# Kernel optimization log

Measured on AMD Instinct MI355X. Metric: run time of the kernel, lower is better.

The kernel has to match this reference:

```python
import jax, jax.numpy as jnp
import numpy as np

K = 20          # neighbors
EPS = 1e-5      # BatchNorm eps (eval mode, running_mean=0, running_var=1)
SLOPE = 0.01    # LeakyReLU default negative_slope


def lrelu(v):
    return jnp.where(v >= 0, v, SLOPE * v)


def bn4d(y, g, b):  # y: (B, C, N, k) or (B, C, N)
    shape = (1, g.shape[0]) + (1,) * (y.ndim - 2)
    return y * (g / jnp.sqrt(1.0 + EPS)).reshape(shape) + b.reshape(shape)


def knn_idx(x, k):  # x: (B, C, N) -> (B, N, k) indices of k nearest points
    xx = jnp.sum(x * x, axis=1)                      # (B, N)
    inner = jnp.einsum('bcn,bcm->bnm', x, x)         # (B, N, N)
    dist = 2.0 * inner - xx[:, :, None] - xx[:, None, :]  # = -||xi-xj||^2
    _, idx = jax.lax.top_k(dist, k)
    return idx


def graph_feature(x, k):  # x: (B, C, N) -> (B, 2C, N, k)
    idx = knn_idx(x, k)                              # (B, N, k)
    xt = jnp.transpose(x, (0, 2, 1))                 # (B, N, C)
    nbr = jax.vmap(lambda p, i: p[i])(xt, idx)       # (B, N, k, C) gather
    ctr = xt[:, :, None, :]                          # (B, N, 1, C)
    feat = jnp.concatenate([nbr - ctr, jnp.broadcast_to(ctr, nbr.shape)], axis=-1)
    return jnp.transpose(feat, (0, 3, 1, 2))         # (B, 2C, N, k)


def edge_conv(x, w, g, b, bias=None):  # 1x1 conv + BN(eval) + LeakyReLU + max over k
    f = graph_feature(x, K)                          # (B, 2C, N, k)
    y = jnp.einsum('oc,bcnk->bonk', w, f)
    if bias is not None:
        y = y + bias.reshape(1, -1, 1, 1)
    return jnp.max(lrelu(bn4d(y, g, b)), axis=-1)    # (B, O, N)


def setup_inputs() -> dict:
    key = jax.random.key(0)
    ks = jax.random.split(key, 24)
    W = lambda k_, o, c: jax.random.normal(k_, (o, c), jnp.float32) / np.sqrt(c)
    g = lambda k_, c: 1.0 + 0.1 * jax.random.normal(k_, (c,), jnp.float32)
    bt = lambda k_, c: 0.1 * jax.random.normal(k_, (c,), jnp.float32)
    return {
        'x': jax.random.normal(ks[0], (8, 1024, 3), jnp.float32),
        'conv1_w': W(ks[1], 64, 6), 'conv1_b': bt(ks[2], 64),
        'bn1_g': g(ks[3], 64), 'bn1_b': bt(ks[4], 64),
        'conv2_w': W(ks[5], 64, 128), 'bn2_g': g(ks[6], 64), 'bn2_b': bt(ks[7], 64),
        'conv3_w': W(ks[8], 128, 128), 'bn3_g': g(ks[9], 128), 'bn3_b': bt(ks[10], 128),
        'conv4_w': W(ks[11], 256, 256), 'bn4_g': g(ks[12], 256), 'bn4_b': bt(ks[13], 256),
        'conv5_w': W(ks[14], 1024, 512),
        'lin1_w': W(ks[15], 512, 1024), 'bn6_g': g(ks[16], 512), 'bn6_b': bt(ks[17], 512),
        'lin2_w': W(ks[18], 256, 512), 'lin2_b': bt(ks[19], 256),
        'bn7_g': g(ks[20], 256), 'bn7_b': bt(ks[21], 256),
        'lin3_w': W(ks[22], 40, 256), 'lin3_b': bt(ks[23], 40),
    }


def reference(x, conv1_w, conv1_b, bn1_g, bn1_b, conv2_w, bn2_g, bn2_b,
              conv3_w, bn3_g, bn3_b, conv4_w, bn4_g, bn4_b, conv5_w,
              lin1_w, bn6_g, bn6_b, lin2_w, lin2_b, bn7_g, bn7_b, lin3_w, lin3_b):
    p = jnp.transpose(x, (0, 2, 1))                  # (B, 3, N)
    x1 = edge_conv(p, conv1_w, bn1_g, bn1_b, bias=conv1_b)   # (B, 64, N)
    x2 = edge_conv(x1, conv2_w, bn2_g, bn2_b)                # (B, 64, N)
    x3 = edge_conv(x2, conv3_w, bn3_g, bn3_b)                # (B, 128, N)
    x4 = edge_conv(x3, conv4_w, bn4_g, bn4_b)                # (B, 256, N)
    xc = jnp.concatenate([x1, x2, x3, x4], axis=1)           # (B, 512, N)
    e = jnp.einsum('oc,bcn->bon', conv5_w, xc)               # (B, 1024, N); bn5 unused in original forward
    gpool = jnp.max(e, axis=-1)                              # (B, 1024) adaptive_max_pool1d(1)
    y = gpool @ lin1_w.T
    y = lrelu(y * (bn6_g / jnp.sqrt(1.0 + EPS)) + bn6_b)     # dropout = identity (eval)
    y = y @ lin2_w.T + lin2_b
    y = lrelu(y * (bn7_g / jnp.sqrt(1.0 + EPS)) + bn7_b)
    return y @ lin3_w.T + lin3_b                             # (B, num_classes)
```

## Files before the change

### kernel.cpp

```cpp
#include <hip/hip_runtime.h>
#include <cmath>
#include <cstdint>
#include <cstddef>

#define NB 8
#define NPTS 1024
#define BN (NB*NPTS)
#define KNN 20
#define XC_C 512
#define BN_SC 0.99999500003749973f

static __device__ __forceinline__ float lrelu(float z) { return z >= 0.f ? z : 0.01f * z; }

template<int CTRL>
static __device__ __forceinline__ void dpp_max2(unsigned& loA, unsigned& hiA,
                                                unsigned& loB, unsigned& hiB) {
    unsigned tlA = (unsigned)__builtin_amdgcn_update_dpp(0, (int)loA, CTRL, 0xF, 0xF, false);
    unsigned thA = (unsigned)__builtin_amdgcn_update_dpp(0, (int)hiA, CTRL, 0xF, 0xF, false);
    unsigned tlB = (unsigned)__builtin_amdgcn_update_dpp(0, (int)loB, CTRL, 0xF, 0xF, false);
    unsigned thB = (unsigned)__builtin_amdgcn_update_dpp(0, (int)hiB, CTRL, 0xF, 0xF, false);
    unsigned long long a = ((unsigned long long)hiA << 32) | loA;
    unsigned long long b = ((unsigned long long)thA << 32) | tlA;
    if (b > a) { loA = tlA; hiA = thA; }
    unsigned long long c = ((unsigned long long)hiB << 32) | loB;
    unsigned long long d = ((unsigned long long)thB << 32) | tlB;
    if (d > c) { loB = tlB; hiB = thB; }
}

static __device__ __forceinline__ void wave_max_u64_x2(unsigned long long vA, unsigned long long vB,
                                                       unsigned long long& winA, unsigned long long& winB) {
    unsigned loA = (unsigned)vA, hiA = (unsigned)(vA >> 32);
    unsigned loB = (unsigned)vB, hiB = (unsigned)(vB >> 32);
    dpp_max2<0x121>(loA, hiA, loB, hiB);
    dpp_max2<0x122>(loA, hiA, loB, hiB);
    dpp_max2<0x124>(loA, hiA, loB, hiB);
    dpp_max2<0x128>(loA, hiA, loB, hiB);
    dpp_max2<0x142>(loA, hiA, loB, hiB);
    dpp_max2<0x143>(loA, hiA, loB, hiB);
    unsigned wloA = (unsigned)__builtin_amdgcn_readlane((int)loA, 63);
    unsigned whiA = (unsigned)__builtin_amdgcn_readlane((int)hiA, 63);
    unsigned wloB = (unsigned)__builtin_amdgcn_readlane((int)loB, 63);
    unsigned whiB = (unsigned)__builtin_amdgcn_readlane((int)hiB, 63);
    winA = ((unsigned long long)whiA << 32) | wloA;
    winB = ((unsigned long long)whiB << 32) | wloB;
}

static __device__ __forceinline__ unsigned long long shflx64(unsigned long long v, int m) {
    int lo = __shfl_xor((int)(unsigned)v, m);
    int hi = __shfl_xor((int)(unsigned)(v >> 32), m);
    return ((unsigned long long)(unsigned)hi << 32) | (unsigned)lo;
}

static __device__ __forceinline__ unsigned long long rdlane64(unsigned long long v, int l) {
    unsigned lo = (unsigned)__builtin_amdgcn_readlane((int)(unsigned)v, l);
    unsigned hi = (unsigned)__builtin_amdgcn_readlane((int)(unsigned)(v >> 32), l);
    return ((unsigned long long)hi << 32) | lo;
}

static __device__ __forceinline__ void bitonic64_desc_x2(unsigned long long& vA,
                                                         unsigned long long& vB, int lane) {
#pragma unroll
    for (int k = 2; k <= 64; k <<= 1) {
#pragma unroll
        for (int j = k >> 1; j > 0; j >>= 1) {
            unsigned long long pA = shflx64(vA, j);
            unsigned long long pB = shflx64(vB, j);
            bool takeMax = (((lane & k) == 0) == ((lane & j) == 0));
            vA = ((pA > vA) == takeMax) ? pA : vA;
            vB = ((pB > vB) == takeMax) ? pB : vB;
        }
    }
}

static __device__ __forceinline__ void select_pair(const float4* accA, const float4* accB,
                                                   const float4* nm4, int lane,
                                                   unsigned long long (*cw)[64],
                                                   int rA, int rB, int* __restrict__ idx) {
    unsigned long long keyA[16], keyB[16];
#pragma unroll
    for (int j = 0; j < 4; j++) {
        float4 nm = nm4[lane + 64*j];
#pragma unroll
        for (int q = 0; q < 4; q++) {
            int m = 4*(lane + 64*j) + q;
            float fA = 2.f * (&accA[j].x)[q] - (&nm.x)[q];
            unsigned uA = __float_as_uint(fA);
            unsigned sA_ = (unsigned)((int)uA >> 31);
            uA ^= (sA_ | 0x80000000u);
            keyA[4*j+q] = ((unsigned long long)uA << 32) | (unsigned)(1023 - m);
            float fB = 2.f * (&accB[j].x)[q] - (&nm.x)[q];
            unsigned uB = __float_as_uint(fB);
            unsigned sB_ = (unsigned)((int)uB >> 31);
            uB ^= (sB_ | 0x80000000u);
            keyB[4*j+q] = ((unsigned long long)uB << 32) | (unsigned)(1023 - m);
        }
    }

    unsigned long long hA = keyA[0], hB = keyB[0];
#pragma unroll
    for (int i = 1; i < 16; i++) {
        hA = keyA[i] > hA ? keyA[i] : hA;
        hB = keyB[i] > hB ? keyB[i] : hB;
    }

    unsigned long long shA = hA, shB = hB;
    bitonic64_desc_x2(shA, shB, lane);
    unsigned long long LA = rdlane64(shA, KNN - 1);
    unsigned long long LB = rdlane64(shB, KNN - 1);

    int cA = 0, cB = 0;
#pragma unroll
    for (int i = 0; i < 16; i++) {
        cA += (keyA[i] >= LA) ? 1 : 0;
        cB += (keyB[i] >= LB) ? 1 : 0;
    }
    int sA = cA, sB = cB;
#pragma unroll
    for (int off = 1; off < 64; off <<= 1) {
        int tA = __shfl_up(sA, off);
        int tB = __shfl_up(sB, off);
        if (lane >= off) { sA += tA; sB += tB; }
    }
    int totA = __builtin_amdgcn_readlane(sA, 63);
    int totB = __builtin_amdgcn_readlane(sB, 63);
    int pA = sA - cA, pB = sB - cB;

    if (totA <= 64 && totB <= 64) {
        int wa = pA, wb = pB;
#pragma unroll
        for (int i = 0; i < 16; i++) {
            if (keyA[i] >= LA) cw[0][wa++] = keyA[i];
            if (keyB[i] >= LB) cw[1][wb++] = keyB[i];
        }
        asm volatile("s_waitcnt lgkmcnt(0)" ::: "memory");
        unsigned long long vA = 0ull, vB = 0ull;
        if (lane < totA) vA = cw[0][lane];
        if (lane < totB) vB = cw[1][lane];
        bitonic64_desc_x2(vA, vB, lane);
        if (lane < KNN) {
            idx[rA * KNN + lane] = 1023 - (int)(unsigned)vA;
            idx[rB * KNN + lane] = 1023 - (int)(unsigned)vB;
        }
    } else {
#pragma unroll
        for (int ksz = 2; ksz <= 16; ksz <<= 1) {
#pragma unroll
            for (int jst = ksz >> 1; jst > 0; jst >>= 1) {
#pragma unroll
                for (int i = 0; i < 16; i++) {
                    int l = i ^ jst;
                    if (l > i) {
                        bool dsc = (i & ksz) == 0;
                        unsigned long long a = keyA[i], bbv = keyA[l];
                        bool swA = dsc ? (a < bbv) : (a > bbv);
                        if (swA) { keyA[i] = bbv; keyA[l] = a; }
                        unsigned long long c = keyB[i], d = keyB[l];
                        bool swB = dsc ? (c < d) : (c > d);
                        if (swB) { keyB[i] = d; keyB[l] = c; }
                    }
                }
            }
        }
        int mineA = 0, mineB = 0;
        for (int kk = 0; kk < KNN; kk++) {
            unsigned long long winA, winB;
            wave_max_u64_x2(keyA[0], keyB[0], winA, winB);
            if (lane == kk) {
                mineA = 1023 - (int)(unsigned)winA;
                mineB = 1023 - (int)(unsigned)winB;
            }
            bool popA = (keyA[0] == winA);
            bool popB = (keyB[0] == winB);
#pragma unroll
            for (int t = 0; t < 15; t++) {
                keyA[t] = popA ? keyA[t+1] : keyA[t];
                keyB[t] = popB ? keyB[t+1] : keyB[t];
            }
            keyA[15] = popA ? 0ull : keyA[15];
            keyB[15] = popB ? 0ull : keyB[15];
        }
        if (lane < KNN) {
            idx[rA * KNN + lane] = mineA;
            idx[rB * KNN + lane] = mineB;
        }
    }
}

static __device__ __forceinline__ unsigned short f2bf(float f) {
    unsigned u = __float_as_uint(f);
    unsigned r = u + 0x7fffu + ((u >> 16) & 1u);
    return (unsigned short)(r >> 16);
}
static __device__ __forceinline__ float bf2f(unsigned short h) {
    return __uint_as_float(((unsigned)h) << 16);
}

typedef __attribute__((ext_vector_type(8))) short short8;
typedef __attribute__((ext_vector_type(4))) float floatx4;

__global__ void prep_k(const float* __restrict__ x, float* __restrict__ ft, float* __restrict__ nrm) {
    int i = blockIdx.x * 256 + threadIdx.x;
    if (i >= BN) return;
    int b = i >> 10, n = i & 1023;
    float a = x[3*i], c = x[3*i+1], d = x[3*i+2];
    float* fb = ft + (size_t)b * 3 * NPTS;
    fb[n] = a; fb[NPTS + n] = c; fb[2*NPTS + n] = d;
    nrm[i] = a*a + c*c + d*d;
}

template<int C, int R>
__global__ __launch_bounds__(256, 2) void knn_k(const float* __restrict__ ft,
                                                const float* __restrict__ frow, int frs,
                                                const float* __restrict__ nrm,
                                                int* __restrict__ idx) {
    __shared__ unsigned long long cand[4][2][64];
    __shared__ float sbuf[2 * 4 * NPTS];
    int tid = threadIdx.x;
    int w = tid >> 6;
    int lane = tid & 63;
    int b    = blockIdx.x & 7;
    int slot = blockIdx.x >> 3;
    int r0 = b * NPTS + slot * (4*R) + R * w;
    const float* ftb = ft + (size_t)b * C * NPTS;

    float4 acc[R][4];
#pragma unroll
    for (int rr = 0; rr < R; rr++)
#pragma unroll
        for (int j = 0; j < 4; j++) acc[rr][j] = make_float4(0.f,0.f,0.f,0.f);

    if constexpr ((C & 3) == 0) {
        constexpr int NC = C / 4;
        const float4* cr0 = (const float4*)(frow + (size_t)r0 * frs);
        int frs4 = frs >> 2;
        const float4* src4 = (const float4*)ftb;
        float* sbase = &sbuf[0];
        float4 pf[4];
#pragma unroll
        for (int i = 0; i < 4; i++) pf[i] = src4[i*256 + tid];
        {
            float4* sw = (float4*)sbase;
#pragma unroll
            for (int i = 0; i < 4; i++) sw[i*256 + tid] = pf[i];
        }
        __syncthreads();
        for (int c4 = 0; c4 < NC; c4++) {
            int cur = c4 & 1;
            if (c4 + 1 < NC) {
#pragma unroll
                for (int i = 0; i < 4; i++) pf[i] = src4[(size_t)(4*(c4+1)+i)*256 + tid];
            }
            float4 ct[R];
#pragma unroll
            for (int rr = 0; rr < R; rr++) ct[rr] = cr0[c4 + rr*frs4];
            const float4* sc = (const float4*)(sbase + cur * 4 * NPTS);
#pragma unroll
            for (int cc = 0; cc < 4; cc++) {
                const float4* rm = sc + cc*256;
#pragma unroll
                for (int j = 0; j < 4; j++) {
                    float4 v = rm[lane + 64*j];
#pragma unroll
                    for (int rr = 0; rr < R; rr++) {
                        float cs = (&ct[rr].x)[cc];
                        acc[rr][j].x = fmaf(cs, v.x, acc[rr][j].x);
                        acc[rr][j].y = fmaf(cs, v.y, acc[rr][j].y);
                        acc[rr][j].z = fmaf(cs, v.z, acc[rr][j].z);
                        acc[rr][j].w = fmaf(cs, v.w, acc[rr][j].w);
                    }
                }
            }
            if (c4 + 1 < NC) {
                float4* sw = (float4*)(sbase + (cur ^ 1) * 4 * NPTS);
#pragma unroll
                for (int i = 0; i < 4; i++) sw[i*256 + tid] = pf[i];
                __syncthreads();
            }
        }
    } else {
        for (int c = 0; c < C; c++) {
            float ct[R];
#pragma unroll
            for (int rr = 0; rr < R; rr++) ct[rr] = frow[(size_t)(r0+rr) * frs + c];
            const float4* rm = (const float4*)(ftb + (size_t)c * NPTS);
#pragma unroll
            for (int j = 0; j < 4; j++) {
                float4 v = rm[lane + 64*j];
#pragma unroll
                for (int rr = 0; rr < R; rr++) {
                    float cs = ct[rr];
                    acc[rr][j].x = fmaf(cs, v.x, acc[rr][j].x);
                    acc[rr][j].y = fmaf(cs, v.y, acc[rr][j].y);
                    acc[rr][j].z = fmaf(cs, v.z, acc[rr][j].z);
                    acc[rr][j].w = fmaf(cs, v.w, acc[rr][j].w);
                }
            }
        }
    }

    const float4* nm4 = (const float4*)(nrm + b * NPTS);
#pragma unroll
    for (int p = 0; p < R/2; p++)
        select_pair(acc[2*p], acc[2*p+1], nm4, lane, cand[w], r0 + 2*p, r0 + 2*p + 1, idx);
}

template<int C, int O, bool HASB, int RPB>
__global__ void hc_k(const float* __restrict__ F, int FS,
                     const float* __restrict__ w, const float* __restrict__ bias,
                     float* __restrict__ Ht, float* __restrict__ Ct) {
    int r0 = blockIdx.x * RPB;
    int o = threadIdx.x;
    const float* wr = w + (size_t)o * (2*C);
    float h[RPB], a2[RPB];
#pragma unroll
    for (int nn = 0; nn < RPB; nn++) { h[nn] = 0.f; a2[nn] = 0.f; }
    if constexpr ((C & 3) == 0) {
        const float4* w1 = (const float4*)wr;
        const float4* w2 = (const float4*)(wr + C);
#pragma unroll 4
        for (int c4 = 0; c4 < C/4; c4++) {
            float4 wa = w1[c4], wb = w2[c4];
#pragma unroll
            for (int nn = 0; nn < RPB; nn++) {
                float4 f = *(const float4*)(F + (size_t)(r0+nn)*FS + 4*c4);
                h[nn]  = fmaf(wa.x,f.x, fmaf(wa.y,f.y, fmaf(wa.z,f.z, fmaf(wa.w,f.w, h[nn]))));
                a2[nn] = fmaf(wb.x,f.x, fmaf(wb.y,f.y, fmaf(wb.z,f.z, fmaf(wb.w,f.w, a2[nn]))));
            }
        }
    } else {
        for (int c = 0; c < C; c++) {
            float wa = wr[c], wb = wr[C+c];
#pragma unroll
            for (int nn = 0; nn < RPB; nn++) {
                float f = F[(size_t)(r0+nn)*FS + c];
                h[nn]  = fmaf(wa, f, h[nn]);
                a2[nn] = fmaf(wb, f, a2[nn]);
            }
        }
    }
    float bs = 0.f;
    if constexpr (HASB) bs = bias[o];
#pragma unroll
    for (int nn = 0; nn < RPB; nn++) {
        size_t ro = (size_t)(r0+nn)*O + o;
        Ht[ro] = h[nn];
        Ct[ro] = a2[nn] - h[nn] + bs;
    }
}

template<int O, bool WFT>
__global__ void gmax_k(const float* __restrict__ Ht, const float* __restrict__ Ct,
                       const int* __restrict__ idx,
                       const float* __restrict__ g, const float* __restrict__ bb,
                       float* __restrict__ xcs, float* __restrict__ ft, float* __restrict__ nrm) {
    int b = blockIdx.x & 7;
    int n = blockIdx.x >> 3;
    int r = b * NPTS + n;
    int o = threadIdx.x;
    const int* id = idx + r * KNN;
    float vmax = -INFINITY, vmin = INFINITY;
    const float* hb = Ht + (size_t)b * NPTS * O + o;
#pragma unroll 4
    for (int k = 0; k < KNN; k++) {
        int m = id[k];
        float v = hb[(size_t)m * O];
        vmax = fmaxf(vmax, v); vmin = fminf(vmin, v);
    }
    float ct = Ct[(size_t)r * O + o];
    float s = g[o] * BN_SC;
    float pre = (s >= 0.f ? vmax : vmin) + ct;
    float out = lrelu(fmaf(s, pre, bb[o]));
    xcs[(size_t)r * XC_C + o] = out;
    if constexpr (WFT) {
        ft[((size_t)b * O + o) * NPTS + n] = out;
        float sq = out * out;
#pragma unroll
        for (int off = 32; off > 0; off >>= 1) sq += __shfl_xor(sq, off);
        __shared__ float red[O/64 > 0 ? O/64 : 1];
        if ((o & 63) == 0) red[o >> 6] = sq;
        __syncthreads();
        if (o == 0) {
            float t = 0.f;
#pragma unroll
            for (int i = 0; i < O/64; i++) t += red[i];
            nrm[r] = t;
        }
    }
}

__global__ void xcvt_k(const float* __restrict__ xc,
                       unsigned short* __restrict__ xh, unsigned short* __restrict__ xl) {
    int i = blockIdx.x * 256 + threadIdx.x;
    float v = xc[i];
    unsigned short h = f2bf(v);
    xh[i] = h;
    xl[i] = f2bf(v - bf2f(h));
}

__global__ void wcvt_k(const float* __restrict__ w5,
                       unsigned short* __restrict__ wh, unsigned short* __restrict__ wl) {
    int i = blockIdx.x * 256 + threadIdx.x;
    float v = w5[i];
    unsigned short h = f2bf(v);
    wh[i] = h;
    wl[i] = f2bf(v - bf2f(h));
}

__global__ __launch_bounds__(256) void conv5mfma_k(const unsigned short* __restrict__ xh,
                                                   const unsigned short* __restrict__ xl,
                                                   const unsigned short* __restrict__ wh,
                                                   const unsigned short* __restrict__ wl,
                                                   float* __restrict__ part) {
    __shared__ short ah_s[32*72];
    __shared__ short al_s[32*72];
    __shared__ short bh_s[128*72];
    __shared__ short bl_s[128*72];
    int b = blockIdx.z, og = blockIdx.y, nt = blockIdx.x;
    int tid = threadIdx.x;
    int w = tid >> 6, lane = tid & 63;
    int m = lane & 15, quad = lane >> 4;
    int h = w >> 1, q = w & 1;
    size_t nbase = (size_t)b * NPTS + nt * 32;
    int obase = og * 128;
    int srow = tid >> 3;
    int scol = (tid & 7) * 8;

    floatx4 acc[4];
#pragma unroll
    for (int t = 0; t < 4; t++) acc[t] = (floatx4){0.f, 0.f, 0.f, 0.f};

    for (int kc = 0; kc < 512; kc += 64) {
        __syncthreads();
        *(short8*)(ah_s + srow*72 + scol) = *(const short8*)(xh + (nbase + srow)*512 + kc + scol);
        *(short8*)(al_s + srow*72 + scol) = *(const short8*)(xl + (nbase + srow)*512 + kc + scol);
#pragma unroll
        for (int i = 0; i < 4; i++) {
            int r = srow + i*32;
            *(short8*)(bh_s + r*72 + scol) = *(const short8*)(wh + (size_t)(obase + r)*512 + kc + scol);
            *(short8*)(bl_s + r*72 + scol) = *(const short8*)(wl + (size_t)(obase + r)*512 + kc + scol);
        }
        __syncthreads();
#pragma unroll
        for (int kk = 0; kk < 2; kk++) {
            short8 ah8 = *(const short8*)(ah_s + (h*16 + m)*72 + kk*32 + quad*8);
            short8 al8 = *(const short8*)(al_s + (h*16 + m)*72 + kk*32 + quad*8);
#pragma unroll
            for (int t = 0; t < 4; t++) {
                short8 bh8 = *(const short8*)(bh_s + (q*64 + t*16 + m)*72 + kk*32 + quad*8);
                short8 bl8 = *(const short8*)(bl_s + (q*64 + t*16 + m)*72 + kk*32 + quad*8);
                acc[t] = __builtin_amdgcn_mfma_f32_16x16x32_bf16(ah8, bh8, acc[t], 0, 0, 0);
                acc[t] = __builtin_amdgcn_mfma_f32_16x16x32_bf16(ah8, bl8, acc[t], 0, 0, 0);
                acc[t] = __builtin_amdgcn_mfma_f32_16x16x32_bf16(al8, bh8, acc[t], 0, 0, 0);
            }
        }
    }
#pragma unroll
    for (int t = 0; t < 4; t++) {
        float v = fmaxf(fmaxf(acc[t][0], acc[t][1]), fmaxf(acc[t][2], acc[t][3]));
        v = fmaxf(v, __shfl_xor(v, 16));
        v = fmaxf(v, __shfl_xor(v, 32));
        if (quad == 0)
            part[((size_t)b * 64 + nt*2 + h) * 1024 + obase + q*64 + t*16 + m] = v;
    }
}

__global__ void gpool_k(const float* __restrict__ part, float* __restrict__ gp) {
    int i = blockIdx.x * 256 + threadIdx.x;
    int b = i >> 10, o = i & 1023;
    const float* pb = part + (size_t)b * 64 * 1024 + o;
    float m = pb[0];
#pragma unroll 4
    for (int j = 1; j < 64; j++) m = fmaxf(m, pb[(size_t)j * 1024]);
    gp[i] = m;
}

template<int C, bool HASBIAS, bool ACT>
__global__ __launch_bounds__(256) void lin_k(const float* __restrict__ X, int xs,
                                             const float* __restrict__ W,
                                             const float* __restrict__ bias,
                                             const float* __restrict__ g, const float* __restrict__ bb,
                                             float* __restrict__ Y, int ys) {
    int wid = (blockIdx.x * 256 + threadIdx.x) >> 6;
    int lane = threadIdx.x & 63;
    int o = wid >> 3;
    int b = wid & 7;
    const float4* wr = (const float4*)(W + (size_t)o * C);
    const float4* xr = (const float4*)(X + (size_t)b * xs);
    float acc = 0.f;
#pragma unroll
    for (int i = 0; i < C/256; i++) {
        float4 w = wr[lane + 64*i];
        float4 xv = xr[lane + 64*i];
        acc = fmaf(w.x,xv.x, fmaf(w.y,xv.y, fmaf(w.z,xv.z, fmaf(w.w,xv.w, acc))));
    }
#pragma unroll
    for (int off = 32; off > 0; off >>= 1) acc += __shfl_xor(acc, off);
    if (lane == 0) {
        if constexpr (HASBIAS) acc += bias[o];
        if constexpr (ACT) acc = lrelu(fmaf(acc, g[o] * BN_SC, bb[o]));
        Y[(size_t)b * ys + o] = acc;
    }
}

extern "C" void kernel_launch(void* const* d_in, const int* in_sizes, int n_in,
                              void* d_out, int out_size, void* d_ws, size_t ws_size,
                              hipStream_t stream) {
    const float* x       = (const float*)d_in[0];
    const float* conv1_w = (const float*)d_in[1];
    const float* conv1_b = (const float*)d_in[2];
    const float* bn1_g   = (const float*)d_in[3];
    const float* bn1_b   = (const float*)d_in[4];
    const float* conv2_w = (const float*)d_in[5];
    const float* bn2_g   = (const float*)d_in[6];
    const float* bn2_b   = (const float*)d_in[7];
    const float* conv3_w = (const float*)d_in[8];
    const float* bn3_g   = (const float*)d_in[9];
    const float* bn3_b   = (const float*)d_in[10];
    const float* conv4_w = (const float*)d_in[11];
    const float* bn4_g   = (const float*)d_in[12];
    const float* bn4_b   = (const float*)d_in[13];
    const float* conv5_w = (const float*)d_in[14];
    const float* lin1_w  = (const float*)d_in[15];
    const float* bn6_g   = (const float*)d_in[16];
    const float* bn6_b   = (const float*)d_in[17];
    const float* lin2_w  = (const float*)d_in[18];
    const float* lin2_b  = (const float*)d_in[19];
    const float* bn7_g   = (const float*)d_in[20];
    const float* bn7_b   = (const float*)d_in[21];
    const float* lin3_w  = (const float*)d_in[22];
    const float* lin3_b  = (const float*)d_in[23];
    float* outp = (float*)d_out;

    float* ws   = (float*)d_ws;
    float* xc   = ws;
    int*   idxb = (int*)(ws + 4194304);
    float* nrm  = ws + 4194304 + 163840;
    float* ft   = nrm + 8192;
    float* part = ft + 1048576;
    float* w5t  = part + 524288;
    float* Ht   = w5t + 524288;
    float* Ct   = Ht + 2097152;
    float* gp   = ft;
    float* y1   = ft + 8192;
    float* y2   = ft + 8192 + 4096;
    unsigned short* xhp = (unsigned short*)Ht;
    unsigned short* xlp = (unsigned short*)Ct;
    unsigned short* whp = (unsigned short*)w5t;
    unsigned short* wlp = whp + 1024*512;

    prep_k<<<BN/256, 256, 0, stream>>>(x, ft, nrm);

    knn_k<3, 4><<<BN/16, 256, 0, stream>>>(ft, x, 3, nrm, idxb);
    hc_k<3, 64, true, 4><<<BN/4, 64, 0, stream>>>(x, 3, conv1_w, conv1_b, Ht, Ct);
    gmax_k<64, true><<<BN, 64, 0, stream>>>(Ht, Ct, idxb, bn1_g, bn1_b, xc + 0, ft, nrm);

    knn_k<64, 4><<<BN/16, 256, 0, stream>>>(ft, xc + 0, XC_C, nrm, idxb);
    hc_k<64, 64, false, 4><<<BN/4, 64, 0, stream>>>(xc + 0, XC_C, conv2_w, nullptr, Ht, Ct);
    gmax_k<64, true><<<BN, 64, 0, stream>>>(Ht, Ct, idxb, bn2_g, bn2_b, xc + 64, ft, nrm);

    knn_k<64, 4><<<BN/16, 256, 0, stream>>>(ft, xc + 64, XC_C, nrm, idxb);
    hc_k<64, 128, false, 4><<<BN/4, 128, 0, stream>>>(xc + 64, XC_C, conv3_w, nullptr, Ht, Ct);
    gmax_k<128, true><<<BN, 128, 0, stream>>>(Ht, Ct, idxb, bn3_g, bn3_b, xc + 128, ft, nrm);

    knn_k<8, 4><<<BN/16, 256, 0, stream>>>(ft, xc + 128, XC_C, nrm, (int*)part);

    knn_k<128, 4><<<BN/16, 256, 0, stream>>>(ft, xc + 128, XC_C, nrm, idxb);
    hc_k<128, 256, false, 8><<<BN/8, 256, 0, stream>>>(xc + 128, XC_C, conv4_w, nullptr, Ht, Ct);
    gmax_k<256, false><<<BN, 256, 0, stream>>>(Ht, Ct, idxb, bn4_g, bn4_b, xc + 256, nullptr, nullptr);

    xcvt_k<<<BN*512/256, 256, 0, stream>>>(xc, xhp, xlp);
    wcvt_k<<<1024*512/256, 256, 0, stream>>>(conv5_w, whp, wlp);
    conv5mfma_k<<<dim3(32, 8, NB), 256, 0, stream>>>(xhp, xlp, whp, wlp, part);
    gpool_k<<<NB*1024/256, 256, 0, stream>>>(part, gp);
    lin_k<1024, false, true><<<NB*512/4, 256, 0, stream>>>(gp, 1024, lin1_w, nullptr, bn6_g, bn6_b, y1, 512);
    lin_k<512,  true,  true><<<NB*256/4, 256, 0, stream>>>(y1, 512, lin2_w, lin2_b, bn7_g, bn7_b, y2, 256);
    lin_k<256,  true, false><<<NB*40/4,  256, 0, stream>>>(y2, 256, lin3_w, lin3_b, nullptr, nullptr, outp, 40);
}
```

Baseline: 417.7 us.

## Double conv5 point tile per block and drop redundant knn launch

Result: slower. 426.1 us (+2.0%).

```diff
diff --git a/kernel.cpp b/kernel.cpp
--- a/kernel.cpp
+++ b/kernel.cpp
@@ -411,8 +411,8 @@
                                                    const unsigned short* __restrict__ wh,
                                                    const unsigned short* __restrict__ wl,
                                                    float* __restrict__ part) {
-    __shared__ short ah_s[32*72];
-    __shared__ short al_s[32*72];
+    __shared__ short ah_s[64*72];
+    __shared__ short al_s[64*72];
     __shared__ short bh_s[128*72];
     __shared__ short bl_s[128*72];
     int b = blockIdx.z, og = blockIdx.y, nt = blockIdx.x;
@@ -420,47 +420,71 @@
     int w = tid >> 6, lane = tid & 63;
     int m = lane & 15, quad = lane >> 4;
     int h = w >> 1, q = w & 1;
-    size_t nbase = (size_t)b * NPTS + nt * 32;
+    size_t nbase = (size_t)b * NPTS + nt * 64;
     int obase = og * 128;
     int srow = tid >> 3;
     int scol = (tid & 7) * 8;
 
-    floatx4 acc[4];
-#pragma unroll
-    for (int t = 0; t < 4; t++) acc[t] = (floatx4){0.f, 0.f, 0.f, 0.f};
+    floatx4 acc[2][4];
+#pragma unroll
+    for (int i = 0; i < 2; i++)
+#pragma unroll
+        for (int t = 0; t < 4; t++) acc[i][t] = (floatx4){0.f, 0.f, 0.f, 0.f};
 
     for (int kc = 0; kc < 512; kc += 64) {
-        __syncthreads();
-        *(short8*)(ah_s + srow*72 + scol) = *(const short8*)(xh + (nbase + srow)*512 + kc + scol);
-        *(short8*)(al_s + srow*72 + scol) = *(const short8*)(xl + (nbase + srow)*512 + kc + scol);
+        short8 pa[4], pb[8];
+        pa[0] = *(const short8*)(xh + (nbase + srow)*512 + kc + scol);
+        pa[1] = *(const short8*)(xl + (nbase + srow)*512 + kc + scol);
+        pa[2] = *(const short8*)(xh + (nbase + 32 + srow)*512 + kc + scol);
+        pa[3] = *(const short8*)(xl + (nbase + 32 + srow)*512 + kc + scol);
 #pragma unroll
         for (int i = 0; i < 4; i++) {
             int r = srow + i*32;
-            *(short8*)(bh_s + r*72 + scol) = *(const short8*)(wh + (size_t)(obase + r)*512 + kc + scol);
-            *(short8*)(bl_s + r*72 + scol) = *(const short8*)(wl + (size_t)(obase + r)*512 + kc + scol);
+            pb[2*i]   = *(const short8*)(wh + (size_t)(obase + r)*512 + kc + scol);
+            pb[2*i+1] = *(const short8*)(wl + (size_t)(obase + r)*512 + kc + scol);
         }
         __syncthreads();
+        *(short8*)(ah_s + srow*72 + scol)      = pa[0];
+        *(short8*)(al_s + srow*72 + scol)      = pa[1];
+        *(short8*)(ah_s + (32+srow)*72 + scol) = pa[2];
+        *(short8*)(al_s + (32+srow)*72 + scol) = pa[3];
+#pragma unroll
+        for (int i = 0; i < 4; i++) {
+            int r = srow + i*32;
+            *(short8*)(bh_s + r*72 + scol) = pb[2*i];
+            *(short8*)(bl_s + r*72 + scol) = pb[2*i+1];
+        }
+        __syncthreads();
 #pragma unroll
         for (int kk = 0; kk < 2; kk++) {
-            short8 ah8 = *(const short8*)(ah_s + (h*16 + m)*72 + kk*32 + quad*8);
-            short8 al8 = *(const short8*)(al_s + (h*16 + m)*72 + kk*32 + quad*8);
+            short8 ah8[2], al8[2];
+#pragma unroll
+            for (int i = 0; i < 2; i++) {
+                ah8[i] = *(const short8*)(ah_s + (i*32 + h*16 + m)*72 + kk*32 + quad*8);
+                al8[i] = *(const short8*)(al_s + (i*32 + h*16 + m)*72 + kk*32 + quad*8);
+            }
 #pragma unroll
             for (int t = 0; t < 4; t++) {
                 short8 bh8 = *(const short8*)(bh_s + (q*64 + t*16 + m)*72 + kk*32 + quad*8);
                 short8 bl8 = *(const short8*)(bl_s + (q*64 + t*16 + m)*72 + kk*32 + quad*8);
-                acc[t] = __builtin_amdgcn_mfma_f32_16x16x32_bf16(ah8, bh8, acc[t], 0, 0, 0);
-                acc[t] = __builtin_amdgcn_mfma_f32_16x16x32_bf16(ah8, bl8, acc[t], 0, 0, 0);
-                acc[t] = __builtin_amdgcn_mfma_f32_16x16x32_bf16(al8, bh8, acc[t], 0, 0, 0);
-            }
-        }
-    }
+#pragma unroll
+                for (int i = 0; i < 2; i++) {
+                    acc[i][t] = __builtin_amdgcn_mfma_f32_16x16x32_bf16(ah8[i], bh8, acc[i][t], 0, 0, 0);
+                    acc[i][t] = __builtin_amdgcn_mfma_f32_16x16x32_bf16(ah8[i], bl8, acc[i][t], 0, 0, 0);
+                    acc[i][t] = __builtin_amdgcn_mfma_f32_16x16x32_bf16(al8[i], bh8, acc[i][t], 0, 0, 0);
+                }
+            }
+        }
+    }
+#pragma unroll
+    for (int i = 0; i < 2; i++)
 #pragma unroll
     for (int t = 0; t < 4; t++) {
-        float v = fmaxf(fmaxf(acc[t][0], acc[t][1]), fmaxf(acc[t][2], acc[t][3]));
+        float v = fmaxf(fmaxf(acc[i][t][0], acc[i][t][1]), fmaxf(acc[i][t][2], acc[i][t][3]));
         v = fmaxf(v, __shfl_xor(v, 16));
         v = fmaxf(v, __shfl_xor(v, 32));
         if (quad == 0)
-            part[((size_t)b * 64 + nt*2 + h) * 1024 + obase + q*64 + t*16 + m] = v;
+            part[((size_t)b * 64 + nt*4 + i*2 + h) * 1024 + obase + q*64 + t*16 + m] = v;
     }
 }
 
@@ -562,15 +586,13 @@
     hc_k<64, 128, false, 4><<<BN/4, 128, 0, stream>>>(xc + 64, XC_C, conv3_w, nullptr, Ht, Ct);
     gmax_k<128, true><<<BN, 128, 0, stream>>>(Ht, Ct, idxb, bn3_g, bn3_b, xc + 128, ft, nrm);
 
-    knn_k<8, 4><<<BN/16, 256, 0, stream>>>(ft, xc + 128, XC_C, nrm, (int*)part);
-
     knn_k<128, 4><<<BN/16, 256, 0, stream>>>(ft, xc + 128, XC_C, nrm, idxb);
     hc_k<128, 256, false, 8><<<BN/8, 256, 0, stream>>>(xc + 128, XC_C, conv4_w, nullptr, Ht, Ct);
     gmax_k<256, false><<<BN, 256, 0, stream>>>(Ht, Ct, idxb, bn4_g, bn4_b, xc + 256, nullptr, nullptr);
 
     xcvt_k<<<BN*512/256, 256, 0, stream>>>(xc, xhp, xlp);
     wcvt_k<<<1024*512/256, 256, 0, stream>>>(conv5_w, whp, wlp);
-    conv5mfma_k<<<dim3(32, 8, NB), 256, 0, stream>>>(xhp, xlp, whp, wlp, part);
+    conv5mfma_k<<<dim3(16, 8, NB), 256, 0, stream>>>(xhp, xlp, whp, wlp, part);
     gpool_k<<<NB*1024/256, 256, 0, stream>>>(part, gp);
     lin_k<1024, false, true><<<NB*512/4, 256, 0, stream>>>(gp, 1024, lin1_w, nullptr, bn6_g, bn6_b, y1, 512);
     lin_k<512,  true,  true><<<NB*256/4, 256, 0, stream>>>(y1, 512, lin2_w, lin2_b, bn7_g, bn7_b, y2, 256);
```
